# Performance work log

Hardware: AMD Instinct MI355X
Metric: run time of the kernel (lower is better)

Reference implementation:

```python
import jax, jax.numpy as jnp
import numpy as np

OUT_FEATURES = 4096
IN_FEATURES = 4096
BLOCK_DIM = 16
K = 64
N_BLOCKS = OUT_FEATURES * IN_FEATURES // BLOCK_DIM  # 1,048,576


def setup_inputs() -> dict:
    key = jax.random.key(0)
    k1, k2, k3, k4, k5, k6 = jax.random.split(key, 6)
    x = jax.random.normal(k1, (8192, IN_FEATURES), dtype=jnp.float32)
    coarse_centroids = jax.random.normal(k2, (K, BLOCK_DIM), dtype=jnp.float32)
    coarse_labels = jax.random.randint(k3, (N_BLOCKS,), 0, K, dtype=jnp.int64)
    res_centroids = jax.random.normal(k4, (K, BLOCK_DIM), dtype=jnp.float32) * 0.1
    res_labels = jax.random.randint(k5, (N_BLOCKS,), 0, K, dtype=jnp.int64)
    bias = jax.random.normal(k6, (OUT_FEATURES,), dtype=jnp.float32)
    return {
        'x': x,
        'coarse_centroids': coarse_centroids,
        'coarse_labels': coarse_labels,
        'res_centroids': res_centroids,
        'res_labels': res_labels,
        'bias': bias,
    }


def _dequantize(coarse_centroids, coarse_labels, res_centroids, res_labels):
    # two-level VQ: coarse lookup + residual correction, per block of BLOCK_DIM
    blocks = coarse_centroids[coarse_labels] + res_centroids[res_labels]  # [N_BLOCKS, BLOCK_DIM]
    return blocks.reshape(OUT_FEATURES, IN_FEATURES)


def reference(x, coarse_centroids, coarse_labels, res_centroids, res_labels, bias):
    W = _dequantize(coarse_centroids, coarse_labels, res_centroids, res_labels)
    # F.linear: x @ W.T + bias
    return jnp.dot(x, W.T) + bias
```

## Files before the change

### kernel.cpp

```cpp
#include <hip/hip_runtime.h>
#include <hip/hip_bf16.h>
#include <stdint.h>

#define M_DIM 8192
#define N_DIM 4096
#define K_DIM 4096
#define BM 256
#define BN 256
#define BK 64
#define NT (K_DIM / BK)
#define THREADS 512
#define NBLOCKS_VQ (N_DIM * K_DIM / 16)

#define ABUF_B 32768
#define BREG   65536
#define SMEM_BYTES 131072

typedef short bf16x8 __attribute__((ext_vector_type(8)));
typedef float f32x4 __attribute__((ext_vector_type(4)));
typedef unsigned short ushort_t;
typedef ushort_t ushort8 __attribute__((ext_vector_type(8)));

#define GLOBAL_AS __attribute__((address_space(1)))
#define LDS_AS __attribute__((address_space(3)))

__device__ __forceinline__ ushort_t f2bf(float f) {
  union { float f; uint32_t u; } v; v.f = f;
  uint32_t u = v.u;
  return (ushort_t)((u + 0x7FFFu + ((u >> 16) & 1u)) >> 16);
}

__global__ __launch_bounds__(256) void dequant_w(
    const float* __restrict__ cc, const int* __restrict__ cl,
    const float* __restrict__ rc, const int* __restrict__ rl,
    ushort_t* __restrict__ wout) {
  int b = blockIdx.x * 256 + threadIdx.x;
  int ci = cl[b];
  int ri = rl[b];
  const float4* c4 = (const float4*)(cc + (size_t)ci * 16);
  const float4* r4 = (const float4*)(rc + (size_t)ri * 16);
  float s[16];
#pragma unroll
  for (int p = 0; p < 4; ++p) {
    float4 a = c4[p];
    float4 r = r4[p];
    s[p * 4 + 0] = a.x + r.x;
    s[p * 4 + 1] = a.y + r.y;
    s[p * 4 + 2] = a.z + r.z;
    s[p * 4 + 3] = a.w + r.w;
  }
  ushort8 o0, o1;
#pragma unroll
  for (int j = 0; j < 8; ++j) o0[j] = f2bf(s[j]);
#pragma unroll
  for (int j = 0; j < 8; ++j) o1[j] = f2bf(s[8 + j]);
  ushort8* dst = (ushort8*)(wout + (size_t)b * 16);
  dst[0] = o0;
  dst[1] = o1;
}

__global__ __launch_bounds__(256) void cvt_x_bf16(const float* __restrict__ x,
                                                  ushort_t* __restrict__ xb) {
  size_t i = (size_t)blockIdx.x * 256 + threadIdx.x;
  const float4* p = (const float4*)x + i * 2;
  float4 a = p[0];
  float4 b = p[1];
  ushort8 o;
  o[0] = f2bf(a.x); o[1] = f2bf(a.y); o[2] = f2bf(a.z); o[3] = f2bf(a.w);
  o[4] = f2bf(b.x); o[5] = f2bf(b.y); o[6] = f2bf(b.z); o[7] = f2bf(b.w);
  ((ushort8*)xb)[i] = o;
}

struct SP {
  const ushort_t* gA;
  const ushort_t* gB;
  char* sm;
  int wuni;
};

__device__ __forceinline__ void stA(const SP& s, int r, int tile, int dbuf) {
  __builtin_amdgcn_global_load_lds(
      (const GLOBAL_AS void*)(s.gA + (size_t)tile * BK + (size_t)r * 64 * K_DIM),
      (LDS_AS void*)(s.sm + dbuf * ABUF_B + r * 8192 + s.wuni), 16, 0, 0);
}
__device__ __forceinline__ void stB(const SP& s, int r, int tile, int dbuf) {
  constexpr int roff[4] = {0, 128, 32, 160};
  __builtin_amdgcn_global_load_lds(
      (const GLOBAL_AS void*)(s.gB + (size_t)tile * BK + (size_t)roff[r] * K_DIM),
      (LDS_AS void*)(s.sm + BREG + dbuf * ABUF_B + r * 8192 + s.wuni), 16, 0, 0);
}

#define BAR()  __builtin_amdgcn_s_barrier()
#define SCB()  __builtin_amdgcn_sched_barrier(0)
#define VMC(n) asm volatile("s_waitcnt vmcnt(" #n ")" ::: "memory")

#define MFMA_Q(ACCM, AARR, BARR, ACCN)                                           \
  __builtin_amdgcn_s_setprio(1);                                                 \
  _Pragma("unroll")                                                              \
  for (int m = 0; m < 4; ++m)                                                    \
    _Pragma("unroll")                                                            \
    for (int ni = 0; ni < 2; ++ni) {                                             \
      acc[ACCM + m][ACCN + ni] = __builtin_amdgcn_mfma_f32_16x16x32_bf16(        \
          AARR[m * 2 + 0], BARR[ni * 2 + 0], acc[ACCM + m][ACCN + ni], 0, 0, 0); \
      acc[ACCM + m][ACCN + ni] = __builtin_amdgcn_mfma_f32_16x16x32_bf16(        \
          AARR[m * 2 + 1], BARR[ni * 2 + 1], acc[ACCM + m][ACCN + ni], 0, 0, 0); \
    }                                                                            \
  __builtin_amdgcn_s_setprio(0);

template<bool ISSUE, bool LAST>
__device__ __forceinline__ void ktile(const SP& sp, int buf, int t,
    int aBase, int bBase, int sw0, int sw1, f32x4 (&acc)[8][4]) {
  const ushort_t* bufA = (const ushort_t*)(sp.sm + buf * ABUF_B);
  const ushort_t* bufB = (const ushort_t*)(sp.sm + BREG + buf * ABUF_B);
  bf16x8 a[8], b0[4], b1[4];

  SCB(); VMC(4); BAR(); SCB();
#pragma unroll
  for (int m = 0; m < 4; ++m) {
    a[m * 2 + 0] = *(const bf16x8*)(bufA + aBase + m * 1024 + sw0);
    a[m * 2 + 1] = *(const bf16x8*)(bufA + aBase + m * 1024 + sw1);
  }
#pragma unroll
  for (int ni = 0; ni < 2; ++ni) {
    b0[ni * 2 + 0] = *(const bf16x8*)(bufB + bBase + ni * 1024 + sw0);
    b0[ni * 2 + 1] = *(const bf16x8*)(bufB + bBase + ni * 1024 + sw1);
  }
  if constexpr (ISSUE) { stA(sp, 0, t + 1, buf ^ 1); stA(sp, 2, t + 1, buf ^ 1); }
  MFMA_Q(0, a, b0, 0);

  SCB();
  if constexpr (LAST) VMC(2); else VMC(4);
  BAR(); SCB();
#pragma unroll
  for (int ni = 0; ni < 2; ++ni) {
    b1[ni * 2 + 0] = *(const bf16x8*)(bufB + bBase + 8192 + ni * 1024 + sw0);
    b1[ni * 2 + 1] = *(const bf16x8*)(bufB + bBase + 8192 + ni * 1024 + sw1);
  }
  if constexpr (ISSUE) { stB(sp, 0, t + 1, buf ^ 1); stB(sp, 1, t + 1, buf ^ 1); }
  MFMA_Q(0, a, b1, 2);

  SCB();
  if constexpr (LAST) VMC(0); else VMC(4);
  BAR(); SCB();
#pragma unroll
  for (int m = 0; m < 4; ++m) {
    a[m * 2 + 0] = *(const bf16x8*)(bufA + aBase + 4096 + m * 1024 + sw0);
    a[m * 2 + 1] = *(const bf16x8*)(bufA + aBase + 4096 + m * 1024 + sw1);
  }
  if constexpr (ISSUE) { stB(sp, 2, t + 1, buf ^ 1); stB(sp, 3, t + 1, buf ^ 1); }
  MFMA_Q(4, a, b0, 0);

  SCB();
  if constexpr (ISSUE) { stA(sp, 1, t + 1, buf ^ 1); stA(sp, 3, t + 1, buf ^ 1); }
  MFMA_Q(4, a, b1, 2);
}

__global__ __launch_bounds__(THREADS, 2) void gemm_bf16(
    const ushort_t* __restrict__ A, const ushort_t* __restrict__ B,
    const float* __restrict__ bias, float* __restrict__ C) {
  extern __shared__ char smem[];

  const int nwg = (M_DIM / BM) * (N_DIM / BN);
  int bid = blockIdx.x;
  int swz = (bid & 7) * (nwg >> 3) + (bid >> 3);
  int bx = swz & 15;
  int by = swz >> 4;
  const int tileM = by * BM;
  const int tileN = bx * BN;

  const int tid = threadIdx.x;
  const int lane = tid & 63;
  const int wave = tid >> 6;
  const int wrM = wave >> 2;
  const int wcN = wave & 3;

  int q = tid >> 3;
  int slot = tid & 7;
  int scol = ((slot ^ (q & 7)) << 3);
  SP sp;
  sp.sm = smem;
  sp.wuni = wave << 10;
  sp.gA = A + (size_t)(tileM + q) * K_DIM + scol;
  int rB0 = ((q >> 5) << 6) + (q & 31);
  sp.gB = B + (size_t)(tileN + rB0) * K_DIM + scol;

  const int lrow = lane & 15;
  const int g = lane >> 4;
  const int l7 = lane & 7;
  const int sw0 = ((g ^ l7) << 3);
  const int sw1 = (((4 + g) ^ l7) << 3);
  const int aBase = (wrM * 128 + lrow) * 64;
  const int bBase = (wcN * 32 + lrow) * 64;

  f32x4 acc[8][4];
#pragma unroll
  for (int m = 0; m < 8; ++m)
#pragma unroll
    for (int n = 0; n < 4; ++n) acc[m][n] = (f32x4)0.0f;

  stA(sp, 0, 0, 0); stA(sp, 2, 0, 0);
  stB(sp, 0, 0, 0); stB(sp, 1, 0, 0);
  stB(sp, 2, 0, 0); stB(sp, 3, 0, 0);
  stA(sp, 1, 0, 0); stA(sp, 3, 0, 0);

  for (int t = 0; t < NT - 1; ++t)
    ktile<true, false>(sp, t & 1, t, aBase, bBase, sw0, sw1, acc);
  ktile<false, true>(sp, (NT - 1) & 1, NT - 1, aBase, bBase, sw0, sw1, acc);

  const int orow = tileM + wrM * 128 + ((lane >> 4) << 2);
  const int ocol0 = tileN + wcN * 64 + lrow;
  float bv[4];
#pragma unroll
  for (int n = 0; n < 4; ++n) bv[n] = bias[ocol0 + n * 16];
#pragma unroll
  for (int m = 0; m < 8; ++m) {
#pragma unroll
    for (int n = 0; n < 4; ++n) {
      size_t base = (size_t)(orow + m * 16) * N_DIM + (ocol0 + n * 16);
#pragma unroll
      for (int r = 0; r < 4; ++r)
        C[base + (size_t)r * N_DIM] = acc[m][n][r] + bv[n];
    }
  }
}

extern "C" void kernel_launch(void* const* d_in, const int* in_sizes, int n_in,
                              void* d_out, int out_size, void* d_ws, size_t ws_size,
                              hipStream_t stream) {
  const float* x = (const float*)d_in[0];
  const float* cc = (const float*)d_in[1];
  const int* cl = (const int*)d_in[2];
  const float* rc = (const float*)d_in[3];
  const int* rl = (const int*)d_in[4];
  const float* bias = (const float*)d_in[5];
  float* out = (float*)d_out;

  ushort_t* Wbf = (ushort_t*)d_ws;
  ushort_t* Xbf = (ushort_t*)d_ws + (size_t)N_DIM * K_DIM;

  (void)hipFuncSetAttribute((const void*)gemm_bf16,
                            hipFuncAttributeMaxDynamicSharedMemorySize, SMEM_BYTES);

  dequant_w<<<NBLOCKS_VQ / 256, 256, 0, stream>>>(cc, cl, rc, rl, Wbf);
  cvt_x_bf16<<<(int)((M_DIM * (size_t)K_DIM / 8) / 256), 256, 0, stream>>>(x, Xbf);
  gemm_bf16<<<(M_DIM / BM) * (N_DIM / BN), THREADS, SMEM_BYTES, stream>>>(Xbf, Wbf, bias, out);
}
```

Before: 266.0 us.

## Collapse per-k-tile interleaved pipeline into one barrier, bulk loads, then MFMAs

Restructures each k-tile iteration of the bf16 GEMM. The old code had four phases with partial vmcnt waits and interleaved LDS reads, global-to-LDS prefetches and MFMA groups. Now it waits for all outstanding loads once and does a single barrier, then reads every A/B fragment for the tile into registers. It then issues all eight prefetches for the next tile and runs all 32 MFMAs back to back. The aim is to cut barrier and waitcnt overhead, at the cost of less overlap between memory and compute and higher register pressure from holding both A halves at once.

```diff
diff --git a/kernel.cpp b/kernel.cpp
--- a/kernel.cpp
+++ b/kernel.cpp
@@ -107,52 +107,48 @@
     }                                                                            \
   __builtin_amdgcn_s_setprio(0);
 
-template<bool ISSUE, bool LAST>
+template<bool ISSUE>
 __device__ __forceinline__ void ktile(const SP& sp, int buf, int t,
     int aBase, int bBase, int sw0, int sw1, f32x4 (&acc)[8][4]) {
   const ushort_t* bufA = (const ushort_t*)(sp.sm + buf * ABUF_B);
   const ushort_t* bufB = (const ushort_t*)(sp.sm + BREG + buf * ABUF_B);
-  bf16x8 a[8], b0[4], b1[4];
-
-  SCB(); VMC(4); BAR(); SCB();
+  bf16x8 a0[8], a1[8], b0[4], b1[4];
+
+  SCB(); VMC(0); BAR(); SCB();
+
 #pragma unroll
   for (int m = 0; m < 4; ++m) {
-    a[m * 2 + 0] = *(const bf16x8*)(bufA + aBase + m * 1024 + sw0);
-    a[m * 2 + 1] = *(const bf16x8*)(bufA + aBase + m * 1024 + sw1);
+    a0[m * 2 + 0] = *(const bf16x8*)(bufA + aBase + m * 1024 + sw0);
+    a0[m * 2 + 1] = *(const bf16x8*)(bufA + aBase + m * 1024 + sw1);
   }
 #pragma unroll
   for (int ni = 0; ni < 2; ++ni) {
     b0[ni * 2 + 0] = *(const bf16x8*)(bufB + bBase + ni * 1024 + sw0);
     b0[ni * 2 + 1] = *(const bf16x8*)(bufB + bBase + ni * 1024 + sw1);
   }
-  if constexpr (ISSUE) { stA(sp, 0, t + 1, buf ^ 1); stA(sp, 2, t + 1, buf ^ 1); }
-  MFMA_Q(0, a, b0, 0);
-
-  SCB();
-  if constexpr (LAST) VMC(2); else VMC(4);
-  BAR(); SCB();
 #pragma unroll
   for (int ni = 0; ni < 2; ++ni) {
     b1[ni * 2 + 0] = *(const bf16x8*)(bufB + bBase + 8192 + ni * 1024 + sw0);
     b1[ni * 2 + 1] = *(const bf16x8*)(bufB + bBase + 8192 + ni * 1024 + sw1);
   }
-  if constexpr (ISSUE) { stB(sp, 0, t + 1, buf ^ 1); stB(sp, 1, t + 1, buf ^ 1); }
-  MFMA_Q(0, a, b1, 2);
-
+#pragma unroll
+  for (int m = 0; m < 4; ++m) {
+    a1[m * 2 + 0] = *(const bf16x8*)(bufA + aBase + 4096 + m * 1024 + sw0);
+    a1[m * 2 + 1] = *(const bf16x8*)(bufA + aBase + 4096 + m * 1024 + sw1);
+  }
+
+  if constexpr (ISSUE) {
+    stA(sp, 0, t + 1, buf ^ 1); stA(sp, 2, t + 1, buf ^ 1);
+    stB(sp, 0, t + 1, buf ^ 1); stB(sp, 1, t + 1, buf ^ 1);
+    stB(sp, 2, t + 1, buf ^ 1); stB(sp, 3, t + 1, buf ^ 1);
+    stA(sp, 1, t + 1, buf ^ 1); stA(sp, 3, t + 1, buf ^ 1);
+  }
   SCB();
-  if constexpr (LAST) VMC(0); else VMC(4);
-  BAR(); SCB();
-#pragma unroll
-  for (int m = 0; m < 4; ++m) {
-    a[m * 2 + 0] = *(const bf16x8*)(bufA + aBase + 4096 + m * 1024 + sw0);
-    a[m * 2 + 1] = *(const bf16x8*)(bufA + aBase + 4096 + m * 1024 + sw1);
-  }
-  if constexpr (ISSUE) { stB(sp, 2, t + 1, buf ^ 1); stB(sp, 3, t + 1, buf ^ 1); }
-  MFMA_Q(4, a, b0, 0);
-
-  SCB();
-  if constexpr (ISSUE) { stA(sp, 1, t + 1, buf ^ 1); stA(sp, 3, t + 1, buf ^ 1); }
-  MFMA_Q(4, a, b1, 2);
+
+  MFMA_Q(0, a0, b0, 0);
+  MFMA_Q(0, a0, b1, 2);
+  MFMA_Q(4, a1, b0, 0);
+  MFMA_Q(4, a1, b1, 2);
 }
 
 __global__ __launch_bounds__(THREADS, 2) void gemm_bf16(
@@ -204,8 +200,8 @@
   stA(sp, 1, 0, 0); stA(sp, 3, 0, 0);
 
   for (int t = 0; t < NT - 1; ++t)
-    ktile<true, false>(sp, t & 1, t, aBase, bBase, sw0, sw1, acc);
-  ktile<false, true>(sp, (NT - 1) & 1, NT - 1, aBase, bBase, sw0, sw1, acc);
+    ktile<true>(sp, t & 1, t, aBase, bBase, sw0, sw1, acc);
+  ktile<false>(sp, (NT - 1) & 1, NT - 1, aBase, bBase, sw0, sw1, acc);
 
   const int orow = tileM + wrM * 128 + ((lane >> 4) << 2);
   const int ocol0 = tileN + wcN * 64 + lrow;
```

Result: no change. 261.5 us (-1.7%).

## Reschedule GEMM k-tile pipeline with ping-pong barriers and reordered prefetch slices

Applied to the files above, without the earlier changes.

Restructures the per-k-tile schedule of the bf16 MFMA GEMM. Next-tile loads now go out in a different order (A slices 1/3 first, then A 0/2, then B), with explicit lgkmcnt waits and barriers around every MFMA quarter, so the waves alternate between LDS reads and matrix math. The vmcnt wait for the next tile moves to the end of each iteration instead of the start. The goal is to hide LDS and global load latency better, at the cost of many more barriers and a tricky dependency on the order in which loads land.

```diff
diff --git a/kernel.cpp b/kernel.cpp
--- a/kernel.cpp
+++ b/kernel.cpp
@@ -12,8 +12,8 @@
 #define THREADS 512
 #define NBLOCKS_VQ (N_DIM * K_DIM / 16)
 
-#define ABUF_B 32768
-#define BREG   65536
+#define ATILE 32768
+#define BREG  65536
 #define SMEM_BYTES 131072
 
 typedef short bf16x8 __attribute__((ext_vector_type(8)));
@@ -81,18 +81,19 @@
 __device__ __forceinline__ void stA(const SP& s, int r, int tile, int dbuf) {
   __builtin_amdgcn_global_load_lds(
       (const GLOBAL_AS void*)(s.gA + (size_t)tile * BK + (size_t)r * 64 * K_DIM),
-      (LDS_AS void*)(s.sm + dbuf * ABUF_B + r * 8192 + s.wuni), 16, 0, 0);
+      (LDS_AS void*)(s.sm + dbuf * ATILE + r * 8192 + s.wuni), 16, 0, 0);
 }
 __device__ __forceinline__ void stB(const SP& s, int r, int tile, int dbuf) {
   constexpr int roff[4] = {0, 128, 32, 160};
   __builtin_amdgcn_global_load_lds(
       (const GLOBAL_AS void*)(s.gB + (size_t)tile * BK + (size_t)roff[r] * K_DIM),
-      (LDS_AS void*)(s.sm + BREG + dbuf * ABUF_B + r * 8192 + s.wuni), 16, 0, 0);
-}
-
-#define BAR()  __builtin_amdgcn_s_barrier()
-#define SCB()  __builtin_amdgcn_sched_barrier(0)
-#define VMC(n) asm volatile("s_waitcnt vmcnt(" #n ")" ::: "memory")
+      (LDS_AS void*)(s.sm + BREG + dbuf * ATILE + r * 8192 + s.wuni), 16, 0, 0);
+}
+
+#define BAR()   __builtin_amdgcn_s_barrier()
+#define SCB()   __builtin_amdgcn_sched_barrier(0)
+#define VMC(n)  asm volatile("s_waitcnt vmcnt(" #n ")" ::: "memory")
+#define LGKM(n) asm volatile("s_waitcnt lgkmcnt(" #n ")" ::: "memory")
 
 #define MFMA_Q(ACCM, AARR, BARR, ACCN)                                           \
   __builtin_amdgcn_s_setprio(1);                                                 \
@@ -107,14 +108,13 @@
     }                                                                            \
   __builtin_amdgcn_s_setprio(0);
 
-template<bool ISSUE, bool LAST>
+template<bool LAST>
 __device__ __forceinline__ void ktile(const SP& sp, int buf, int t,
     int aBase, int bBase, int sw0, int sw1, f32x4 (&acc)[8][4]) {
-  const ushort_t* bufA = (const ushort_t*)(sp.sm + buf * ABUF_B);
-  const ushort_t* bufB = (const ushort_t*)(sp.sm + BREG + buf * ABUF_B);
+  const ushort_t* bufA = (const ushort_t*)(sp.sm + buf * ATILE);
+  const ushort_t* bufB = (const ushort_t*)(sp.sm + BREG + buf * ATILE);
   bf16x8 a[8], b0[4], b1[4];
 
-  SCB(); VMC(4); BAR(); SCB();
 #pragma unroll
   for (int m = 0; m < 4; ++m) {
     a[m * 2 + 0] = *(const bf16x8*)(bufA + aBase + m * 1024 + sw0);
@@ -125,34 +125,40 @@
     b0[ni * 2 + 0] = *(const bf16x8*)(bufB + bBase + ni * 1024 + sw0);
     b0[ni * 2 + 1] = *(const bf16x8*)(bufB + bBase + ni * 1024 + sw1);
   }
-  if constexpr (ISSUE) { stA(sp, 0, t + 1, buf ^ 1); stA(sp, 2, t + 1, buf ^ 1); }
+  if constexpr (!LAST) { stA(sp, 1, t + 1, buf ^ 1); stA(sp, 3, t + 1, buf ^ 1); }
+  LGKM(8); SCB();
+  BAR(); LGKM(0); SCB();
   MFMA_Q(0, a, b0, 0);
-
-  SCB();
-  if constexpr (LAST) VMC(2); else VMC(4);
-  BAR(); SCB();
+  if constexpr (!LAST) VMC(2); else VMC(0);
+  BAR(); SCB();
+
 #pragma unroll
   for (int ni = 0; ni < 2; ++ni) {
     b1[ni * 2 + 0] = *(const bf16x8*)(bufB + bBase + 8192 + ni * 1024 + sw0);
     b1[ni * 2 + 1] = *(const bf16x8*)(bufB + bBase + 8192 + ni * 1024 + sw1);
   }
-  if constexpr (ISSUE) { stB(sp, 0, t + 1, buf ^ 1); stB(sp, 1, t + 1, buf ^ 1); }
+  if constexpr (!LAST) { stA(sp, 0, t + 1, buf ^ 1); stA(sp, 2, t + 1, buf ^ 1); }
+  BAR(); LGKM(0); SCB();
   MFMA_Q(0, a, b1, 2);
-
-  SCB();
-  if constexpr (LAST) VMC(0); else VMC(4);
-  BAR(); SCB();
+  BAR(); SCB();
+
 #pragma unroll
   for (int m = 0; m < 4; ++m) {
     a[m * 2 + 0] = *(const bf16x8*)(bufA + aBase + 4096 + m * 1024 + sw0);
     a[m * 2 + 1] = *(const bf16x8*)(bufA + aBase + 4096 + m * 1024 + sw1);
   }
-  if constexpr (ISSUE) { stB(sp, 2, t + 1, buf ^ 1); stB(sp, 3, t + 1, buf ^ 1); }
+  if constexpr (!LAST) { stB(sp, 0, t + 1, buf ^ 1); stB(sp, 1, t + 1, buf ^ 1); }
+  BAR(); LGKM(0); SCB();
   MFMA_Q(4, a, b0, 0);
-
-  SCB();
-  if constexpr (ISSUE) { stA(sp, 1, t + 1, buf ^ 1); stA(sp, 3, t + 1, buf ^ 1); }
+  BAR(); SCB();
+
+  if constexpr (!LAST) {
+    stB(sp, 2, t + 1, buf ^ 1); stB(sp, 3, t + 1, buf ^ 1);
+    SCB(); VMC(2);
+  }
+  BAR();
   MFMA_Q(4, a, b1, 2);
+  BAR(); SCB();
 }
 
 __global__ __launch_bounds__(THREADS, 2) void gemm_bf16(
@@ -200,12 +206,13 @@
 
   stA(sp, 0, 0, 0); stA(sp, 2, 0, 0);
   stB(sp, 0, 0, 0); stB(sp, 1, 0, 0);
+  stA(sp, 1, 0, 0); stA(sp, 3, 0, 0);
   stB(sp, 2, 0, 0); stB(sp, 3, 0, 0);
-  stA(sp, 1, 0, 0); stA(sp, 3, 0, 0);
+  SCB(); VMC(4); BAR(); SCB();
 
   for (int t = 0; t < NT - 1; ++t)
-    ktile<true, false>(sp, t & 1, t, aBase, bBase, sw0, sw1, acc);
-  ktile<false, true>(sp, (NT - 1) & 1, NT - 1, aBase, bBase, sw0, sw1, acc);
+    ktile<false>(sp, t & 1, t, aBase, bBase, sw0, sw1, acc);
+  ktile<true>(sp, (NT - 1) & 1, NT - 1, aBase, bBase, sw0, sw1, acc);
 
   const int orow = tileM + wrM * 128 + ((lane >> 4) << 2);
   const int ocol0 = tileN + wcN * 64 + lrow;
```

Measured after the change: 281.0 us. 1.06x slower.
